# Optimization experiments

Hardware: AMD Instinct MI355X
Metric: run time of the kernel (lower is better)

The kernel has to match this reference:

```python
import jax, jax.numpy as jnp
import numpy as np

D_X, D_Y, HIDDEN, K = 256, 32, 256, 2
T = 50
SIG_MIN, SIG_MAX = 0.002, 1.0
N = 4096
D_XY = D_X + D_Y
D_IN = D_XY + 2 * HIDDEN  # 800


def setup_inputs() -> dict:
    key = jax.random.key(0)
    ks = jax.random.split(key, 12)
    def w(k, shape, fan):
        return (jax.random.normal(k, shape, jnp.float32) / np.sqrt(fan)).astype(jnp.float32)
    return {
        "xy0": jax.random.normal(ks[0], (N, D_XY), jnp.float32) * SIG_MAX,  # randn * sigma_max * extra_noise(=1)
        "t0": jax.random.randint(ks[1], (N,), 0, K),
        "t_embed": w(ks[2], (K, HIDDEN), 1),
        "tm_w1": w(ks[3], (1, HIDDEN), 1), "tm_b1": jnp.zeros((HIDDEN,), jnp.float32),
        "tm_w2": w(ks[4], (HIDDEN, HIDDEN), HIDDEN), "tm_b2": jnp.zeros((HIDDEN,), jnp.float32),
        "tr_w1": w(ks[5], (D_IN, HIDDEN), D_IN), "tr_b1": jnp.zeros((HIDDEN,), jnp.float32),
        "tr_w2": w(ks[6], (HIDDEN, HIDDEN), HIDDEN), "tr_b2": jnp.zeros((HIDDEN,), jnp.float32),
        "sh_w": w(ks[7], (HIDDEN, D_XY), HIDDEN), "sh_b": jnp.zeros((D_XY,), jnp.float32),
        "ch_w": w(ks[8], (HIDDEN, K), HIDDEN), "ch_b": jnp.zeros((K,), jnp.float32),
    }


def _sigma(t):
    return SIG_MIN * (SIG_MAX / SIG_MIN) ** t


def reference(xy0, t0, t_embed, tm_w1, tm_b1, tm_w2, tm_b2,
              tr_w1, tr_b1, tr_w2, tr_b2, sh_w, sh_b, ch_w, ch_b):
    n = xy0.shape[0]
    silu = jax.nn.silu
    base_key = jax.random.key(42)

    def net(xy, t, tau):
        te = t_embed[t]  # (n, H) embedding lookup
        # time_mlp on scalar tau -> (H,), broadcast over batch (tau is identical per row)
        tm = silu(tau * tm_w1[0] + tm_b1) @ tm_w2 + tm_b2
        tm = jnp.broadcast_to(tm, (n, HIDDEN))
        h = jnp.concatenate([xy, te, tm], axis=-1)  # (n, D_IN)
        h = silu(silu(h @ tr_w1 + tr_b1) @ tr_w2 + tr_b2)
        return h @ sh_w + sh_b, h @ ch_w + ch_b  # score (n, D_XY), logits (n, K)

    def body(carry, t_idx):
        xy, t = carry
        tau = t_idx.astype(jnp.float32) / T
        sig_t = _sigma(tau)
        sig_prev = _sigma((t_idx - 1).astype(jnp.float32) / T)
        step = sig_t ** 2 - sig_prev ** 2  # positive reverse-SDE step size
        score, logits = net(xy, t, tau)
        k1, k2 = jax.random.split(jax.random.fold_in(base_key, t_idx))
        xy = xy + step * score + jnp.sqrt(step) * jax.random.normal(k1, xy.shape, xy.dtype)
        t = jax.random.categorical(k2, logits, axis=-1)  # multinomial(softmax(logits), 1)
        return (xy, t), None

    steps = jnp.arange(T - 1, 0, -1)  # reversed(range(1, T))
    (xy, t), _ = jax.lax.scan(body, (xy0, t0), steps)
    return xy[:, :D_X], xy[:, D_X:], t
```

## Files before the change

### kernel.cpp

```cpp
#include <hip/hip_runtime.h>
#include <math.h>


#define DXY 288
#define HID 256
#define NTHR 512
#define XYP 296
#define HP  264
#define OUT_Y_OFF 1048576
#define OUT_T_OFF 1179648
#define STEP_OFF 25600
#define WS_SWE 25728

typedef unsigned int u32;

__device__ __forceinline__ void tf2x32(u32 k0, u32 k1, u32 x0, u32 x1, u32& o0, u32& o1) {
  u32 ks2 = k0 ^ k1 ^ 0x1BD11BDAu;
#define TFR(r) { x0 += x1; x1 = (x1 << (r)) | (x1 >> (32 - (r))); x1 ^= x0; }
  x0 += k0; x1 += k1;
  TFR(13) TFR(15) TFR(26) TFR(6)
  x0 += k1;  x1 += ks2 + 1u;
  TFR(17) TFR(29) TFR(16) TFR(24)
  x0 += ks2; x1 += k0 + 2u;
  TFR(13) TFR(15) TFR(26) TFR(6)
  x0 += k0;  x1 += k1 + 3u;
  TFR(17) TFR(29) TFR(16) TFR(24)
  x0 += k1;  x1 += ks2 + 4u;
  TFR(13) TFR(15) TFR(26) TFR(6)
  x0 += ks2; x1 += k0 + 5u;
#undef TFR
  o0 = x0; o1 = x1;
}

__device__ __forceinline__ u32 pbits(u32 ka, u32 kb, u32 j) {
  u32 w0, w1;
  tf2x32(ka, kb, 0u, j, w0, w1);
  return w0 ^ w1;
}

__device__ __forceinline__ float u01f(u32 bits) {
  union { u32 i; float f; } v;
  v.i = (bits >> 9) | 0x3F800000u;
  return v.f - 1.0f;
}

__device__ __forceinline__ float erfinv32(float x) {
  float w = -log1pf(-x * x);
  float p;
  if (w < 5.0f) {
    w -= 2.5f;
    p = 2.81022636e-08f;
    p = fmaf(p, w, 3.43273939e-07f);
    p = fmaf(p, w, -3.5233877e-06f);
    p = fmaf(p, w, -4.39150654e-06f);
    p = fmaf(p, w, 0.00021858087f);
    p = fmaf(p, w, -0.00125372503f);
    p = fmaf(p, w, -0.00417768164f);
    p = fmaf(p, w, 0.246640727f);
    p = fmaf(p, w, 1.50140941f);
  } else {
    w = sqrtf(w) - 3.0f;
    p = -0.000200214257f;
    p = fmaf(p, w, 0.000100950558f);
    p = fmaf(p, w, 0.00134934322f);
    p = fmaf(p, w, -0.00367342844f);
    p = fmaf(p, w, 0.00573950773f);
    p = fmaf(p, w, -0.0076224613f);
    p = fmaf(p, w, 0.00943887047f);
    p = fmaf(p, w, 1.00167406f);
    p = fmaf(p, w, 2.83297682f);
  }
  return p * x;
}

__device__ __forceinline__ float nrmf(u32 bits) {
  float val = fmaf(u01f(bits), 2.0f, -0.99999994f);
  return 1.41421356f * erfinv32(val);
}
__device__ __forceinline__ float gumf(u32 bits) {
  float u = fmaxf(u01f(bits), 1.17549435e-38f);
  return -logf(-logf(u));
}
__device__ __forceinline__ float siluf(float x) {
  return x / (1.0f + expf(-x));
}

struct B8 { float4 a0, a1, a2, a3, b0, b1, b2, b3; };

__device__ __forceinline__ void fma8x4(float acc[4], const float4 x0, const float4 x1, const B8& B) {
  acc[0]=fmaf(x0.x,B.a0.x,acc[0]); acc[1]=fmaf(x0.x,B.a0.y,acc[1]); acc[2]=fmaf(x0.x,B.a0.z,acc[2]); acc[3]=fmaf(x0.x,B.a0.w,acc[3]);
  acc[0]=fmaf(x0.y,B.a1.x,acc[0]); acc[1]=fmaf(x0.y,B.a1.y,acc[1]); acc[2]=fmaf(x0.y,B.a1.z,acc[2]); acc[3]=fmaf(x0.y,B.a1.w,acc[3]);
  acc[0]=fmaf(x0.z,B.a2.x,acc[0]); acc[1]=fmaf(x0.z,B.a2.y,acc[1]); acc[2]=fmaf(x0.z,B.a2.z,acc[2]); acc[3]=fmaf(x0.z,B.a2.w,acc[3]);
  acc[0]=fmaf(x0.w,B.a3.x,acc[0]); acc[1]=fmaf(x0.w,B.a3.y,acc[1]); acc[2]=fmaf(x0.w,B.a3.z,acc[2]); acc[3]=fmaf(x0.w,B.a3.w,acc[3]);
  acc[0]=fmaf(x1.x,B.b0.x,acc[0]); acc[1]=fmaf(x1.x,B.b0.y,acc[1]); acc[2]=fmaf(x1.x,B.b0.z,acc[2]); acc[3]=fmaf(x1.x,B.b0.w,acc[3]);
  acc[0]=fmaf(x1.y,B.b1.x,acc[0]); acc[1]=fmaf(x1.y,B.b1.y,acc[1]); acc[2]=fmaf(x1.y,B.b1.z,acc[2]); acc[3]=fmaf(x1.y,B.b1.w,acc[3]);
  acc[0]=fmaf(x1.z,B.b2.x,acc[0]); acc[1]=fmaf(x1.z,B.b2.y,acc[1]); acc[2]=fmaf(x1.z,B.b2.z,acc[2]); acc[3]=fmaf(x1.z,B.b2.w,acc[3]);
  acc[0]=fmaf(x1.w,B.b3.x,acc[0]); acc[1]=fmaf(x1.w,B.b3.y,acc[1]); acc[2]=fmaf(x1.w,B.b3.z,acc[2]); acc[3]=fmaf(x1.w,B.b3.w,acc[3]);
}

__device__ __forceinline__ void gll16(const float* g, float* l) {
  __builtin_amdgcn_global_load_lds((const __attribute__((address_space(1))) void*)g,
                                   (__attribute__((address_space(3))) void*)l, 16, 0, 0);
}

__device__ __forceinline__ void issue_stage(int seq, float* buf, int tid,
                                            const float* w1, const float* w2,
                                            const float* sw) {
  if (seq < 17) {
    const float* src = (seq < 9) ? (w1 + seq * 8192) : (w2 + (seq - 9) * 8192);
    #pragma unroll
    for (int j = 0; j < 4; ++j) {
      int u = j * 512 + tid;
      gll16(src + u * 4, buf + u * 4);
    }
  } else {
    const int t0 = (seq - 17) * 32;
    #pragma unroll
    for (int j = 0; j < 4; ++j) {
      int u = j * 512 + tid;
      int r = u >> 6, c4 = (u & 63) << 2;
      gll16(sw + (t0 + r) * DXY + c4, buf + u * 4);
    }
  }
}

__device__ __forceinline__ void tile_mm(float accA[4], float accB[4],
                                        const float* tile, const float* aA,
                                        const float* aB, int cg) {
  #pragma unroll
  for (int kk = 0; kk < 32; kk += 8) {
    const float* tp = tile + kk * 256 + cg;
    B8 B;
    B.a0 = *(const float4*)(tp);
    B.a1 = *(const float4*)(tp + 256);
    B.a2 = *(const float4*)(tp + 512);
    B.a3 = *(const float4*)(tp + 768);
    B.b0 = *(const float4*)(tp + 1024);
    B.b1 = *(const float4*)(tp + 1280);
    B.b2 = *(const float4*)(tp + 1536);
    B.b3 = *(const float4*)(tp + 1792);
    float4 xA0 = *(const float4*)(aA + kk), xA1 = *(const float4*)(aA + kk + 4);
    float4 xB0 = *(const float4*)(aB + kk), xB1 = *(const float4*)(aB + kk + 4);
    fma8x4(accA, xA0, xA1, B);
    fma8x4(accB, xB0, xB1, B);
  }
}

#define WAIT_TILE() do { \
  asm volatile("s_waitcnt vmcnt(4)" ::: "memory"); \
  __builtin_amdgcn_s_barrier(); \
  __builtin_amdgcn_sched_barrier(0); } while (0)

#define DONE_TILE() do { \
  asm volatile("s_waitcnt lgkmcnt(0)" ::: "memory"); \
  __builtin_amdgcn_s_barrier(); \
  __builtin_amdgcn_sched_barrier(0); } while (0)

__global__ void precompute_ct(
    const float* __restrict__ t_embed,
    const float* __restrict__ tm_w1, const float* __restrict__ tm_b1,
    const float* __restrict__ tm_w2, const float* __restrict__ tm_b2,
    const float* __restrict__ tr_w1, const float* __restrict__ tr_b1,
    float* __restrict__ ws)
{
  const int t = blockIdx.x + 1;
  const int c = threadIdx.x;
  __shared__ float tmpre[HID];
  __shared__ float tmv[HID];
  const float tau = (float)t / 50.0f;

  tmpre[c] = siluf(fmaf(tau, tm_w1[c], tm_b1[c]));
  __syncthreads();
  {
    float acc = tm_b2[c];
    for (int i = 0; i < HID; i++)
      acc = fmaf(tmpre[i], tm_w2[i * HID + c], acc);
    tmv[c] = acc;
  }
  __syncthreads();
  float D = 0.f;
  for (int i = 0; i < HID; i++)
    D = fmaf(tmv[i], tr_w1[(544 + i) * HID + c], D);
  float ce0 = tr_b1[c], ce1 = tr_b1[c];
  for (int i = 0; i < HID; i++) {
    ce0 = fmaf(t_embed[i], tr_w1[(288 + i) * HID + c], ce0);
    ce1 = fmaf(t_embed[HID + i], tr_w1[(288 + i) * HID + c], ce1);
  }
  ws[t * 512 + c] = ce0 + D;
  ws[t * 512 + 256 + c] = ce1 + D;

  if (c == 0) {
    const double lt = 6.214608098422191;
    float sig_t = (float)(0.002 * exp(((double)t / 50.0) * lt));
    float sig_p = (float)(0.002 * exp(((double)(t - 1) / 50.0) * lt));
    float stepf = sig_t * sig_t - sig_p * sig_p;
    ws[STEP_OFF + 2 * t] = stepf;
    ws[STEP_OFF + 2 * t + 1] = sqrtf(stepf);
  }
}

__global__ void transpose_swe(const float* __restrict__ sw, float* __restrict__ ws)
{
  int i = blockIdx.x * 256 + threadIdx.x;
  int c = i >> 8, k = i & 255;
  ws[WS_SWE + c * 256 + k] = sw[k * DXY + 256 + c];
}

__global__ __launch_bounds__(NTHR, 2) void sampler_k(
    const float* __restrict__ xy0, const int* __restrict__ t0,
    const float* __restrict__ tr_w1,
    const float* __restrict__ tr_w2, const float* __restrict__ tr_b2,
    const float* __restrict__ sh_w, const float* __restrict__ sh_b,
    const float* __restrict__ ch_w, const float* __restrict__ ch_b,
    const float* __restrict__ ws,
    float* __restrict__ out)
{
  __shared__ float wt[2][8192];
  __shared__ float wext[8192];
  __shared__ float xy_s[16][XYP];
  __shared__ float h1_s[16][HP];
  __shared__ float h2_s[16][HP];
  __shared__ int tcur_s[16];

  const int tid = threadIdx.x;
  const int lane = tid & 63;
  const int w = tid >> 6;
  const int row0g = blockIdx.x * 16;

  const int r0 = lane >> 3;
  const int r1 = r0 + 8;
  const int cg = w * 32 + (lane & 7) * 4;
  const int rE = lane >> 2;
  const int cEl = w * 4 + (lane & 3);

  issue_stage(0, wt[0], tid, tr_w1, tr_w2, sh_w);
  issue_stage(1, wt[1], tid, tr_w1, tr_w2, sh_w);

  for (int idx = tid; idx < 16 * (DXY / 4); idx += NTHR) {
    int r = idx / (DXY / 4);
    int q = idx - r * (DXY / 4);
    *(float4*)&xy_s[r][q * 4] = *(const float4*)(xy0 + (row0g + r) * DXY + q * 4);
  }
  for (int i = tid; i < 8192; i += NTHR) wext[i] = ws[WS_SWE + i];
  if (tid < 16) tcur_s[tid] = t0[row0g + tid];

  float chw0[4], chw1[4];
  #pragma unroll
  for (int j = 0; j < 4; j++) {
    chw0[j] = ch_w[(lane * 4 + j) * 2 + 0];
    chw1[j] = ch_w[(lane * 4 + j) * 2 + 1];
  }
  const float4 b2r = *(const float4*)(tr_b2 + cg);
  const float cb0 = ch_b[0], cb1 = ch_b[1];
  const float4 sbm = *(const float4*)(sh_b + cg);
  const float sbE = sh_b[256 + cEl];
  const float* epb = wext + cEl * 256;
  __syncthreads();

  int pp = 0;

  #pragma unroll 1
  for (int t_idx = 49; t_idx >= 1; --t_idx) {
    const float stepf = ws[STEP_OFF + 2 * t_idx];
    const float sstep = ws[STEP_OFF + 2 * t_idx + 1];

    u32 f0, f1, k1a, k1b, k2a, k2b;
    tf2x32(0u, 42u, 0u, (u32)t_idx, f0, f1);
    tf2x32(f0, f1, 0u, 0u, k1a, k1b);
    tf2x32(f0, f1, 0u, 1u, k2a, k2b);

    {
      float accA[4] = {0.f, 0.f, 0.f, 0.f};
      float accB[4] = {0.f, 0.f, 0.f, 0.f};
      #pragma unroll 1
      for (int s = 0; s < 9; ++s) {
        WAIT_TILE();
        tile_mm(accA, accB, wt[pp], &xy_s[r0][s * 32], &xy_s[r1][s * 32], cg);
        if (s == 8) {
          const int tc0 = tcur_s[r0], tc1 = tcur_s[r1];
          const float* ct = ws + t_idx * 512;
          const float4 ctA = *(const float4*)(ct + tc0 * 256 + cg);
          const float4 ctB = *(const float4*)(ct + tc1 * 256 + cg);
          float4 oA, oB;
          oA.x = siluf(accA[0] + ctA.x); oA.y = siluf(accA[1] + ctA.y);
          oA.z = siluf(accA[2] + ctA.z); oA.w = siluf(accA[3] + ctA.w);
          oB.x = siluf(accB[0] + ctB.x); oB.y = siluf(accB[1] + ctB.y);
          oB.z = siluf(accB[2] + ctB.z); oB.w = siluf(accB[3] + ctB.w);
          *(float4*)&h1_s[r0][cg] = oA;
          *(float4*)&h1_s[r1][cg] = oB;
        }
        DONE_TILE();
        issue_stage(s + 2, wt[pp], tid, tr_w1, tr_w2, sh_w);
        pp ^= 1;
      }
    }

    {
      float accA[4] = {0.f, 0.f, 0.f, 0.f};
      float accB[4] = {0.f, 0.f, 0.f, 0.f};
      #pragma unroll 1
      for (int s = 0; s < 8; ++s) {
        WAIT_TILE();
        tile_mm(accA, accB, wt[pp], &h1_s[r0][s * 32], &h1_s[r1][s * 32], cg);
        if (s == 7) {
          float4 oA, oB;
          oA.x = siluf(accA[0] + b2r.x); oA.y = siluf(accA[1] + b2r.y);
          oA.z = siluf(accA[2] + b2r.z); oA.w = siluf(accA[3] + b2r.w);
          oB.x = siluf(accB[0] + b2r.x); oB.y = siluf(accB[1] + b2r.y);
          oB.z = siluf(accB[2] + b2r.z); oB.w = siluf(accB[3] + b2r.w);
          *(float4*)&h2_s[r0][cg] = oA;
          *(float4*)&h2_s[r1][cg] = oB;
        }
        DONE_TILE();
        issue_stage(s + 11, wt[pp], tid, tr_w1, tr_w2, sh_w);
        pp ^= 1;
      }
    }

    {
      float4 hL0 = *(const float4*)&h2_s[2 * w][lane * 4];
      float4 hL1 = *(const float4*)&h2_s[2 * w + 1][lane * 4];
      float pA0 = hL0.x * chw0[0] + hL0.y * chw0[1] + hL0.z * chw0[2] + hL0.w * chw0[3];
      float pA1 = hL0.x * chw1[0] + hL0.y * chw1[1] + hL0.z * chw1[2] + hL0.w * chw1[3];
      float pB0 = hL1.x * chw0[0] + hL1.y * chw0[1] + hL1.z * chw0[2] + hL1.w * chw0[3];
      float pB1 = hL1.x * chw1[0] + hL1.y * chw1[1] + hL1.z * chw1[2] + hL1.w * chw1[3];
      #pragma unroll
      for (int off = 32; off > 0; off >>= 1) {
        pA0 += __shfl_xor(pA0, off);
        pA1 += __shfl_xor(pA1, off);
        pB0 += __shfl_xor(pB0, off);
        pB1 += __shfl_xor(pB1, off);
      }
      u32 grow = (u32)(row0g + 2 * w + ((lane >> 1) & 1));
      float g = gumf(pbits(k2a, k2b, grow * 2u + (u32)(lane & 1)));
      float g0 = __shfl(g, 0), g1 = __shfl(g, 1);
      float g2 = __shfl(g, 2), g3 = __shfl(g, 3);
      if (lane == 0) {
        tcur_s[2 * w]     = (pA1 + cb1 + g1 > pA0 + cb0 + g0) ? 1 : 0;
        tcur_s[2 * w + 1] = (pB1 + cb1 + g3 > pB0 + cb0 + g2) ? 1 : 0;
      }
    }

    {
      float accA[4] = {0.f, 0.f, 0.f, 0.f};
      float accB[4] = {0.f, 0.f, 0.f, 0.f};
      #pragma unroll 1
      for (int s = 0; s < 8; ++s) {
        WAIT_TILE();
        tile_mm(accA, accB, wt[pp], &h2_s[r0][s * 32], &h2_s[r1][s * 32], cg);
        if (s == 7) {
          const u32 jA = (u32)(row0g + r0) * 288u + (u32)cg;
          const u32 jB = (u32)(row0g + r1) * 288u + (u32)cg;
          float4 xA = *(const float4*)&xy_s[r0][cg];
          float4 xB = *(const float4*)&xy_s[r1][cg];
          xA.x = fmaf(sstep, nrmf(pbits(k1a, k1b, jA + 0u)), fmaf(stepf, accA[0] + sbm.x, xA.x));
          xA.y = fmaf(sstep, nrmf(pbits(k1a, k1b, jA + 1u)), fmaf(stepf, accA[1] + sbm.y, xA.y));
          xA.z = fmaf(sstep, nrmf(pbits(k1a, k1b, jA + 2u)), fmaf(stepf, accA[2] + sbm.z, xA.z));
          xA.w = fmaf(sstep, nrmf(pbits(k1a, k1b, jA + 3u)), fmaf(stepf, accA[3] + sbm.w, xA.w));
          xB.x = fmaf(sstep, nrmf(pbits(k1a, k1b, jB + 0u)), fmaf(stepf, accB[0] + sbm.x, xB.x));
          xB.y = fmaf(sstep, nrmf(pbits(k1a, k1b, jB + 1u)), fmaf(stepf, accB[1] + sbm.y, xB.y));
          xB.z = fmaf(sstep, nrmf(pbits(k1a, k1b, jB + 2u)), fmaf(stepf, accB[2] + sbm.z, xB.z));
          xB.w = fmaf(sstep, nrmf(pbits(k1a, k1b, jB + 3u)), fmaf(stepf, accB[3] + sbm.w, xB.w));
          *(float4*)&xy_s[r0][cg] = xA;
          *(float4*)&xy_s[r1][cg] = xB;
          float sE0 = 0.f, sE1 = 0.f;
          #pragma unroll 4
          for (int k = 0; k < 256; k += 8) {
            float4 h0  = *(const float4*)&h2_s[rE][k];
            float4 h1v = *(const float4*)&h2_s[rE][k + 4];
            float4 wa = *(const float4*)(epb + k);
            float4 wb = *(const float4*)(epb + k + 4);
            sE0 = fmaf(h0.w, wa.w, fmaf(h0.z, wa.z, fmaf(h0.y, wa.y, fmaf(h0.x, wa.x, sE0))));
            sE1 = fmaf(h1v.w, wb.w, fmaf(h1v.z, wb.z, fmaf(h1v.y, wb.y, fmaf(h1v.x, wb.x, sE1))));
          }
          float sE = sE0 + sE1;
          u32 jE = (u32)(row0g + rE) * 288u + (u32)(256 + cEl);
          float nE = nrmf(pbits(k1a, k1b, jE));
          xy_s[rE][256 + cEl] = fmaf(sstep, nE, fmaf(stepf, sE + sbE, xy_s[rE][256 + cEl]));
        }
        DONE_TILE();
        int nxt = s + 19;
        if (nxt >= 25) nxt -= 25;
        issue_stage(nxt, wt[pp], tid, tr_w1, tr_w2, sh_w);
        pp ^= 1;
      }
    }
  }

  for (int idx = tid; idx < 16 * 64; idx += NTHR) {
    int r = idx >> 6;
    int c4 = (idx & 63) * 4;
    *(float4*)(out + (row0g + r) * 256 + c4) = *(const float4*)&xy_s[r][c4];
  }
  for (int idx = tid; idx < 16 * 8; idx += NTHR) {
    int r = idx >> 3;
    int c4 = (idx & 7) * 4;
    *(float4*)(out + OUT_Y_OFF + (row0g + r) * 32 + c4) = *(const float4*)&xy_s[r][256 + c4];
  }
  if (tid < 16) out[OUT_T_OFF + row0g + tid] = (float)tcur_s[tid];
}

extern "C" void kernel_launch(void* const* d_in, const int* in_sizes, int n_in,
                              void* d_out, int out_size, void* d_ws, size_t ws_size,
                              hipStream_t stream) {
  (void)in_sizes; (void)n_in; (void)ws_size; (void)out_size;
  const float* xy0     = (const float*)d_in[0];
  const int*   t0      = (const int*)d_in[1];
  const float* t_embed = (const float*)d_in[2];
  const float* tm_w1   = (const float*)d_in[3];
  const float* tm_b1   = (const float*)d_in[4];
  const float* tm_w2   = (const float*)d_in[5];
  const float* tm_b2   = (const float*)d_in[6];
  const float* tr_w1   = (const float*)d_in[7];
  const float* tr_b1   = (const float*)d_in[8];
  const float* tr_w2   = (const float*)d_in[9];
  const float* tr_b2   = (const float*)d_in[10];
  const float* sh_w    = (const float*)d_in[11];
  const float* sh_b    = (const float*)d_in[12];
  const float* ch_w    = (const float*)d_in[13];
  const float* ch_b    = (const float*)d_in[14];
  float* ws  = (float*)d_ws;
  float* out = (float*)d_out;

  precompute_ct<<<49, 256, 0, stream>>>(t_embed, tm_w1, tm_b1, tm_w2, tm_b2,
                                        tr_w1, tr_b1, ws);
  transpose_swe<<<32, 256, 0, stream>>>(sh_w, ws);
  sampler_k<<<256, NTHR, 0, stream>>>(xy0, t0, tr_w1, tr_w2, tr_b2,
                                      sh_w, sh_b, ch_w, ch_b, ws, out);
}
```

Measured before the change: 2.227 ms.

## Triple-buffer weight tiles with one barrier per tile and hoisted epilogues

Replaces the double-buffered weight-tile pipeline, which needed two barriers per tile, with a three-slot ring buffer. Each tile now needs one barrier and issues the next prefetch before its compute. The extra 32 KB of shared memory comes from dropping the shared copy of the extended score-head weights, which are now read straight from global workspace. The activation epilogues move out of the tile loops, the ct load is hoisted, and the categorical sampling now overlaps the first tile of the last GEMM. Padding also shrinks, so LDS bank behaviour and the latency of reading the epilogue weights from global may change.

```diff
diff --git a/kernel.cpp b/kernel.cpp
--- a/kernel.cpp
+++ b/kernel.cpp
@@ -5,8 +5,8 @@
 #define DXY 288
 #define HID 256
 #define NTHR 512
-#define XYP 296
-#define HP  264
+#define XYP 292
+#define HP  260
 #define OUT_Y_OFF 1048576
 #define OUT_T_OFF 1179648
 #define STEP_OFF 25600
@@ -146,15 +146,12 @@
   }
 }
 
-#define WAIT_TILE() do { \
-  asm volatile("s_waitcnt vmcnt(4)" ::: "memory"); \
-  __builtin_amdgcn_s_barrier(); \
-  __builtin_amdgcn_sched_barrier(0); } while (0)
-
-#define DONE_TILE() do { \
-  asm volatile("s_waitcnt lgkmcnt(0)" ::: "memory"); \
-  __builtin_amdgcn_s_barrier(); \
-  __builtin_amdgcn_sched_barrier(0); } while (0)
+__device__ __forceinline__ void tile_sync() {
+  asm volatile("s_waitcnt vmcnt(4)" ::: "memory");
+  asm volatile("s_waitcnt lgkmcnt(0)" ::: "memory");
+  __builtin_amdgcn_s_barrier();
+  __builtin_amdgcn_sched_barrier(0);
+}
 
 __global__ void precompute_ct(
     const float* __restrict__ t_embed,
@@ -215,8 +212,7 @@
     const float* __restrict__ ws,
     float* __restrict__ out)
 {
-  __shared__ float wt[2][8192];
-  __shared__ float wext[8192];
+  __shared__ float wt[3][8192];
   __shared__ float xy_s[16][XYP];
   __shared__ float h1_s[16][HP];
   __shared__ float h2_s[16][HP];
@@ -241,7 +237,6 @@
     int q = idx - r * (DXY / 4);
     *(float4*)&xy_s[r][q * 4] = *(const float4*)(xy0 + (row0g + r) * DXY + q * 4);
   }
-  for (int i = tid; i < 8192; i += NTHR) wext[i] = ws[WS_SWE + i];
   if (tid < 16) tcur_s[tid] = t0[row0g + tid];
 
   float chw0[4], chw1[4];
@@ -254,10 +249,12 @@
   const float cb0 = ch_b[0], cb1 = ch_b[1];
   const float4 sbm = *(const float4*)(sh_b + cg);
   const float sbE = sh_b[256 + cEl];
-  const float* epb = wext + cEl * 256;
+  const float* epb = ws + WS_SWE + cEl * 256;
   __syncthreads();
 
-  int pp = 0;
+  int q = 0;
+  int cur = 0;
+  int gb = 2;
 
   #pragma unroll 1
   for (int t_idx = 49; t_idx >= 1; --t_idx) {
@@ -268,31 +265,32 @@
     tf2x32(0u, 42u, 0u, (u32)t_idx, f0, f1);
     tf2x32(f0, f1, 0u, 0u, k1a, k1b);
     tf2x32(f0, f1, 0u, 1u, k2a, k2b);
+
+    const int tc0 = tcur_s[r0], tc1 = tcur_s[r1];
+    const float* ctp = ws + t_idx * 512;
+    const float4 ctA = *(const float4*)(ctp + tc0 * 256 + cg);
+    const float4 ctB = *(const float4*)(ctp + tc1 * 256 + cg);
 
     {
       float accA[4] = {0.f, 0.f, 0.f, 0.f};
       float accB[4] = {0.f, 0.f, 0.f, 0.f};
       #pragma unroll 1
       for (int s = 0; s < 9; ++s) {
-        WAIT_TILE();
-        tile_mm(accA, accB, wt[pp], &xy_s[r0][s * 32], &xy_s[r1][s * 32], cg);
-        if (s == 8) {
-          const int tc0 = tcur_s[r0], tc1 = tcur_s[r1];
-          const float* ct = ws + t_idx * 512;
-          const float4 ctA = *(const float4*)(ct + tc0 * 256 + cg);
-          const float4 ctB = *(const float4*)(ct + tc1 * 256 + cg);
-          float4 oA, oB;
-          oA.x = siluf(accA[0] + ctA.x); oA.y = siluf(accA[1] + ctA.y);
-          oA.z = siluf(accA[2] + ctA.z); oA.w = siluf(accA[3] + ctA.w);
-          oB.x = siluf(accB[0] + ctB.x); oB.y = siluf(accB[1] + ctB.y);
-          oB.z = siluf(accB[2] + ctB.z); oB.w = siluf(accB[3] + ctB.w);
-          *(float4*)&h1_s[r0][cg] = oA;
-          *(float4*)&h1_s[r1][cg] = oB;
-        }
-        DONE_TILE();
-        issue_stage(s + 2, wt[pp], tid, tr_w1, tr_w2, sh_w);
-        pp ^= 1;
+        tile_sync();
+        int nx = q + 2; if (nx >= 25) nx -= 25;
+        issue_stage(nx, wt[gb], tid, tr_w1, tr_w2, sh_w);
+        tile_mm(accA, accB, wt[cur], &xy_s[r0][s * 32], &xy_s[r1][s * 32], cg);
+        q = (q + 1 == 25) ? 0 : q + 1;
+        cur = (cur + 1 == 3) ? 0 : cur + 1;
+        gb = (gb + 1 == 3) ? 0 : gb + 1;
       }
+      float4 oA, oB;
+      oA.x = siluf(accA[0] + ctA.x); oA.y = siluf(accA[1] + ctA.y);
+      oA.z = siluf(accA[2] + ctA.z); oA.w = siluf(accA[3] + ctA.w);
+      oB.x = siluf(accB[0] + ctB.x); oB.y = siluf(accB[1] + ctB.y);
+      oB.z = siluf(accB[2] + ctB.z); oB.w = siluf(accB[3] + ctB.w);
+      *(float4*)&h1_s[r0][cg] = oA;
+      *(float4*)&h1_s[r1][cg] = oB;
     }
 
     {
@@ -300,45 +298,21 @@
       float accB[4] = {0.f, 0.f, 0.f, 0.f};
       #pragma unroll 1
       for (int s = 0; s < 8; ++s) {
-        WAIT_TILE();
-        tile_mm(accA, accB, wt[pp], &h1_s[r0][s * 32], &h1_s[r1][s * 32], cg);
-        if (s == 7) {
-          float4 oA, oB;
-          oA.x = siluf(accA[0] + b2r.x); oA.y = siluf(accA[1] + b2r.y);
-          oA.z = siluf(accA[2] + b2r.z); oA.w = siluf(accA[3] + b2r.w);
-          oB.x = siluf(accB[0] + b2r.x); oB.y = siluf(accB[1] + b2r.y);
-          oB.z = siluf(accB[2] + b2r.z); oB.w = siluf(accB[3] + b2r.w);
-          *(float4*)&h2_s[r0][cg] = oA;
-          *(float4*)&h2_s[r1][cg] = oB;
-        }
-        DONE_TILE();
-        issue_stage(s + 11, wt[pp], tid, tr_w1, tr_w2, sh_w);
-        pp ^= 1;
+        tile_sync();
+        int nx = q + 2; if (nx >= 25) nx -= 25;
+        issue_stage(nx, wt[gb], tid, tr_w1, tr_w2, sh_w);
+        tile_mm(accA, accB, wt[cur], &h1_s[r0][s * 32], &h1_s[r1][s * 32], cg);
+        q = (q + 1 == 25) ? 0 : q + 1;
+        cur = (cur + 1 == 3) ? 0 : cur + 1;
+        gb = (gb + 1 == 3) ? 0 : gb + 1;
       }
-    }
-
-    {
-      float4 hL0 = *(const float4*)&h2_s[2 * w][lane * 4];
-      float4 hL1 = *(const float4*)&h2_s[2 * w + 1][lane * 4];
-      float pA0 = hL0.x * chw0[0] + hL0.y * chw0[1] + hL0.z * chw0[2] + hL0.w * chw0[3];
-      float pA1 = hL0.x * chw1[0] + hL0.y * chw1[1] + hL0.z * chw1[2] + hL0.w * chw1[3];
-      float pB0 = hL1.x * chw0[0] + hL1.y * chw0[1] + hL1.z * chw0[2] + hL1.w * chw0[3];
-      float pB1 = hL1.x * chw1[0] + hL1.y * chw1[1] + hL1.z * chw1[2] + hL1.w * chw1[3];
-      #pragma unroll
-      for (int off = 32; off > 0; off >>= 1) {
-        pA0 += __shfl_xor(pA0, off);
-        pA1 += __shfl_xor(pA1, off);
-        pB0 += __shfl_xor(pB0, off);
-        pB1 += __shfl_xor(pB1, off);
-      }
-      u32 grow = (u32)(row0g + 2 * w + ((lane >> 1) & 1));
-      float g = gumf(pbits(k2a, k2b, grow * 2u + (u32)(lane & 1)));
-      float g0 = __shfl(g, 0), g1 = __shfl(g, 1);
-      float g2 = __shfl(g, 2), g3 = __shfl(g, 3);
-      if (lane == 0) {
-        tcur_s[2 * w]     = (pA1 + cb1 + g1 > pA0 + cb0 + g0) ? 1 : 0;
-        tcur_s[2 * w + 1] = (pB1 + cb1 + g3 > pB0 + cb0 + g2) ? 1 : 0;
-      }
+      float4 oA, oB;
+      oA.x = siluf(accA[0] + b2r.x); oA.y = siluf(accA[1] + b2r.y);
+      oA.z = siluf(accA[2] + b2r.z); oA.w = siluf(accA[3] + b2r.w);
+      oB.x = siluf(accB[0] + b2r.x); oB.y = siluf(accB[1] + b2r.y);
+      oB.z = siluf(accB[2] + b2r.z); oB.w = siluf(accB[3] + b2r.w);
+      *(float4*)&h2_s[r0][cg] = oA;
+      *(float4*)&h2_s[r1][cg] = oB;
     }
 
     {
@@ -346,46 +320,70 @@
       float accB[4] = {0.f, 0.f, 0.f, 0.f};
       #pragma unroll 1
       for (int s = 0; s < 8; ++s) {
-        WAIT_TILE();
-        tile_mm(accA, accB, wt[pp], &h2_s[r0][s * 32], &h2_s[r1][s * 32], cg);
-        if (s == 7) {
-          const u32 jA = (u32)(row0g + r0) * 288u + (u32)cg;
-          const u32 jB = (u32)(row0g + r1) * 288u + (u32)cg;
-          float4 xA = *(const float4*)&xy_s[r0][cg];
-          float4 xB = *(const float4*)&xy_s[r1][cg];
-          xA.x = fmaf(sstep, nrmf(pbits(k1a, k1b, jA + 0u)), fmaf(stepf, accA[0] + sbm.x, xA.x));
-          xA.y = fmaf(sstep, nrmf(pbits(k1a, k1b, jA + 1u)), fmaf(stepf, accA[1] + sbm.y, xA.y));
-          xA.z = fmaf(sstep, nrmf(pbits(k1a, k1b, jA + 2u)), fmaf(stepf, accA[2] + sbm.z, xA.z));
-          xA.w = fmaf(sstep, nrmf(pbits(k1a, k1b, jA + 3u)), fmaf(stepf, accA[3] + sbm.w, xA.w));
-          xB.x = fmaf(sstep, nrmf(pbits(k1a, k1b, jB + 0u)), fmaf(stepf, accB[0] + sbm.x, xB.x));
-          xB.y = fmaf(sstep, nrmf(pbits(k1a, k1b, jB + 1u)), fmaf(stepf, accB[1] + sbm.y, xB.y));
-          xB.z = fmaf(sstep, nrmf(pbits(k1a, k1b, jB + 2u)), fmaf(stepf, accB[2] + sbm.z, xB.z));
-          xB.w = fmaf(sstep, nrmf(pbits(k1a, k1b, jB + 3u)), fmaf(stepf, accB[3] + sbm.w, xB.w));
-          *(float4*)&xy_s[r0][cg] = xA;
-          *(float4*)&xy_s[r1][cg] = xB;
-          float sE0 = 0.f, sE1 = 0.f;
-          #pragma unroll 4
-          for (int k = 0; k < 256; k += 8) {
-            float4 h0  = *(const float4*)&h2_s[rE][k];
-            float4 h1v = *(const float4*)&h2_s[rE][k + 4];
-            float4 wa = *(const float4*)(epb + k);
-            float4 wb = *(const float4*)(epb + k + 4);
-            sE0 = fmaf(h0.w, wa.w, fmaf(h0.z, wa.z, fmaf(h0.y, wa.y, fmaf(h0.x, wa.x, sE0))));
-            sE1 = fmaf(h1v.w, wb.w, fmaf(h1v.z, wb.z, fmaf(h1v.y, wb.y, fmaf(h1v.x, wb.x, sE1))));
+        tile_sync();
+        int nx = q + 2; if (nx >= 25) nx -= 25;
+        issue_stage(nx, wt[gb], tid, tr_w1, tr_w2, sh_w);
+        if (s == 0) {
+          float4 hL0 = *(const float4*)&h2_s[2 * w][lane * 4];
+          float4 hL1 = *(const float4*)&h2_s[2 * w + 1][lane * 4];
+          float pA0 = hL0.x * chw0[0] + hL0.y * chw0[1] + hL0.z * chw0[2] + hL0.w * chw0[3];
+          float pA1 = hL0.x * chw1[0] + hL0.y * chw1[1] + hL0.z * chw1[2] + hL0.w * chw1[3];
+          float pB0 = hL1.x * chw0[0] + hL1.y * chw0[1] + hL1.z * chw0[2] + hL1.w * chw0[3];
+          float pB1 = hL1.x * chw1[0] + hL1.y * chw1[1] + hL1.z * chw1[2] + hL1.w * chw1[3];
+          #pragma unroll
+          for (int off = 32; off > 0; off >>= 1) {
+            pA0 += __shfl_xor(pA0, off);
+            pA1 += __shfl_xor(pA1, off);
+            pB0 += __shfl_xor(pB0, off);
+            pB1 += __shfl_xor(pB1, off);
           }
-          float sE = sE0 + sE1;
-          u32 jE = (u32)(row0g + rE) * 288u + (u32)(256 + cEl);
-          float nE = nrmf(pbits(k1a, k1b, jE));
-          xy_s[rE][256 + cEl] = fmaf(sstep, nE, fmaf(stepf, sE + sbE, xy_s[rE][256 + cEl]));
+          u32 grow = (u32)(row0g + 2 * w + ((lane >> 1) & 1));
+          float g = gumf(pbits(k2a, k2b, grow * 2u + (u32)(lane & 1)));
+          float g0 = __shfl(g, 0), g1 = __shfl(g, 1);
+          float g2 = __shfl(g, 2), g3 = __shfl(g, 3);
+          if (lane == 0) {
+            tcur_s[2 * w]     = (pA1 + cb1 + g1 > pA0 + cb0 + g0) ? 1 : 0;
+            tcur_s[2 * w + 1] = (pB1 + cb1 + g3 > pB0 + cb0 + g2) ? 1 : 0;
+          }
         }
-        DONE_TILE();
-        int nxt = s + 19;
-        if (nxt >= 25) nxt -= 25;
-        issue_stage(nxt, wt[pp], tid, tr_w1, tr_w2, sh_w);
-        pp ^= 1;
+        tile_mm(accA, accB, wt[cur], &h2_s[r0][s * 32], &h2_s[r1][s * 32], cg);
+        q = (q + 1 == 25) ? 0 : q + 1;
+        cur = (cur + 1 == 3) ? 0 : cur + 1;
+        gb = (gb + 1 == 3) ? 0 : gb + 1;
       }
+      const u32 jA = (u32)(row0g + r0) * 288u + (u32)cg;
+      const u32 jB = (u32)(row0g + r1) * 288u + (u32)cg;
+      float4 xA = *(const float4*)&xy_s[r0][cg];
+      float4 xB = *(const float4*)&xy_s[r1][cg];
+      xA.x = fmaf(sstep, nrmf(pbits(k1a, k1b, jA + 0u)), fmaf(stepf, accA[0] + sbm.x, xA.x));
+      xA.y = fmaf(sstep, nrmf(pbits(k1a, k1b, jA + 1u)), fmaf(stepf, accA[1] + sbm.y, xA.y));
+      xA.z = fmaf(sstep, nrmf(pbits(k1a, k1b, jA + 2u)), fmaf(stepf, accA[2] + sbm.z, xA.z));
+      xA.w = fmaf(sstep, nrmf(pbits(k1a, k1b, jA + 3u)), fmaf(stepf, accA[3] + sbm.w, xA.w));
+      xB.x = fmaf(sstep, nrmf(pbits(k1a, k1b, jB + 0u)), fmaf(stepf, accB[0] + sbm.x, xB.x));
+      xB.y = fmaf(sstep, nrmf(pbits(k1a, k1b, jB + 1u)), fmaf(stepf, accB[1] + sbm.y, xB.y));
+      xB.z = fmaf(sstep, nrmf(pbits(k1a, k1b, jB + 2u)), fmaf(stepf, accB[2] + sbm.z, xB.z));
+      xB.w = fmaf(sstep, nrmf(pbits(k1a, k1b, jB + 3u)), fmaf(stepf, accB[3] + sbm.w, xB.w));
+      *(float4*)&xy_s[r0][cg] = xA;
+      *(float4*)&xy_s[r1][cg] = xB;
+
+      float sE0 = 0.f, sE1 = 0.f;
+      #pragma unroll 4
+      for (int k = 0; k < 256; k += 8) {
+        float4 h0  = *(const float4*)&h2_s[rE][k];
+        float4 h1v = *(const float4*)&h2_s[rE][k + 4];
+        float4 wa = *(const float4*)(epb + k);
+        float4 wb = *(const float4*)(epb + k + 4);
+        sE0 = fmaf(h0.w, wa.w, fmaf(h0.z, wa.z, fmaf(h0.y, wa.y, fmaf(h0.x, wa.x, sE0))));
+        sE1 = fmaf(h1v.w, wb.w, fmaf(h1v.z, wb.z, fmaf(h1v.y, wb.y, fmaf(h1v.x, wb.x, sE1))));
+      }
+      float sE = sE0 + sE1;
+      u32 jE = (u32)(row0g + rE) * 288u + (u32)(256 + cEl);
+      float nE = nrmf(pbits(k1a, k1b, jE));
+      xy_s[rE][256 + cEl] = fmaf(sstep, nE, fmaf(stepf, sE + sbE, xy_s[rE][256 + cEl]));
     }
   }
+
+  __syncthreads();
 
   for (int idx = tid; idx < 16 * 64; idx += NTHR) {
     int r = idx >> 6;
```

New measurement: 2.556 ms. 1.15x slower.
